# Kernel optimization log

Measured on AMD Instinct MI355X. Metric: run time of the kernel, lower is better.

## Reference

```python
import jax, jax.numpy as jnp
import numpy as np
import math

D = 256   # d_model / hidden_size
Q = 256   # q_num (query-side nodes)
K = 512   # k_num (key-side nodes)
NEG = -9e15


def _forward(q_enc, k_enc, rel_k, rel_v, k_adj,
             W_glob, b_glob, W_gv0, b_gv0, W_gv1, b_gv1,
             W_gq, b_gq, W_lq, b_lq,
             W_locgate, b_locgate, W_gate, b_gate):
    d = q_enc.shape[-1]
    scale = 1.0 / math.sqrt(d)
    act = jnp.tanh  # activation_func='tanh'

    # --- global sigmoid blending of k_enc with the mean query encoding ---
    q_glob_enc = jnp.mean(q_enc, axis=0)                       # [d]
    k_s = jax.nn.sigmoid((q_glob_enc @ W_glob + b_glob) @ k_enc.T * scale)  # [K]
    k_s = k_s[:, None]                                         # [K,1]
    g_1 = q_glob_enc @ W_gv0 + b_gv0                           # [d]
    k_1 = k_enc @ W_gv1 + b_gv1                                # [K,d]
    k_enc2 = (1.0 - k_s) * k_1 + k_s * g_1                     # [K,d]

    # --- global relation-aware attention over k nodes ---
    q_glob = q_enc @ W_gq + b_gq                               # [Q,d]
    qk_logit = q_glob @ k_enc2.T                               # [Q,K]
    qk_r = jnp.einsum('qd,qkd->qk', q_glob, rel_k)             # [Q,K]
    glob_attn = jax.nn.softmax(act((qk_logit + qk_r) * scale), axis=-1)  # [Q,K]

    # --- local adjacency-masked attention ---
    q_loc = q_enc @ W_lq + b_lq                                # [Q,d]
    qnk_logit = q_loc @ k_enc2.T                               # [Q,K]
    qnk_r = jnp.einsum('qd,qkd->qk', q_loc, rel_k)             # [Q,K]
    loc_attn = act((qnk_logit + qnk_r) * scale)                # [Q,K]
    # loc_weight_rep[q,i,j] = loc_attn[q,j]  (repeat + view in torch)
    mask = (k_adj != 0)[None, :, :]                            # [1,K,K]
    masked = jnp.where(mask, loc_attn[:, None, :], NEG)        # [Q,K,K]
    attn_adj_norm = jax.nn.softmax(masked, axis=-1)            # [Q,K,K]
    k_loc = jnp.einsum('qij,jd->qid', attn_adj_norm, k_enc2)   # [Q,K,d]

    # --- local gate between neighborhood value and self value ---
    # sigmoid(cat([k_loc, k_self]) @ W_locgate + b); k_self is broadcast k_enc2
    Wg1, Wg2 = W_locgate[:d], W_locgate[d:]                    # [d,1] each
    gate_logit = (jnp.einsum('qid,d->qi', k_loc, Wg1[:, 0])
                  + (k_enc2 @ Wg2)[None, :, 0] + b_locgate[0])  # [Q,K]
    loc_gate = jax.nn.sigmoid(gate_logit)[..., None]           # [Q,K,1]
    k_awr = loc_gate * k_loc + (1.0 - loc_gate) * k_enc2[None, :, :]  # [Q,K,d]

    # --- aggregate with global attention + relation values ---
    k_matmul = jnp.einsum('qk,qkd->qd', glob_attn, k_awr)      # [Q,d]
    k_r_matmul = jnp.einsum('qk,qkd->qd', glob_attn, rel_v)    # [Q,d]
    q_enc_new = k_matmul + k_r_matmul                          # [Q,d]

    # --- residual gate ---
    Wq1, Wq2 = W_gate[:d], W_gate[d:]
    gate = jax.nn.sigmoid(q_enc_new @ Wq1 + q_enc @ Wq2 + b_gate)  # [Q,1]
    h = gate * q_enc_new + (1.0 - gate) * q_enc                # [Q,d]
    return h


def setup_inputs() -> dict:
    key = jax.random.key(0)
    ks = jax.random.split(key, 16)
    def w(k, shape):
        return jax.random.normal(k, shape, jnp.float32) * 0.02
    return {
        'q_enc': jax.random.normal(ks[0], (Q, D), jnp.float32),
        'k_enc': jax.random.normal(ks[1], (K, D), jnp.float32),
        'rel_k': jax.random.normal(ks[2], (Q, K, D), jnp.float32) * 0.1,
        'rel_v': jax.random.normal(ks[3], (Q, K, D), jnp.float32) * 0.1,
        'k_adj': jax.random.randint(ks[4], (K, K), 0, 2, jnp.int64) if jax.config.jax_enable_x64 else jax.random.randint(ks[4], (K, K), 0, 2, jnp.int32),
        'W_glob': w(ks[5], (D, D)), 'b_glob': jnp.zeros((D,), jnp.float32),
        'W_gv0': w(ks[6], (D, D)), 'b_gv0': jnp.zeros((D,), jnp.float32),
        'W_gv1': w(ks[7], (D, D)), 'b_gv1': jnp.zeros((D,), jnp.float32),
        'W_gq': w(ks[8], (D, D)), 'b_gq': jnp.zeros((D,), jnp.float32),
        'W_lq': w(ks[9], (D, D)), 'b_lq': jnp.zeros((D,), jnp.float32),
        'W_locgate': w(ks[10], (2 * D, 1)), 'b_locgate': jnp.zeros((1,), jnp.float32),
        'W_gate': w(ks[11], (2 * D, 1)), 'b_gate': jnp.zeros((1,), jnp.float32),
    }


def reference(q_enc, k_enc, rel_k, rel_v, k_adj,
              W_glob, b_glob, W_gv0, b_gv0, W_gv1, b_gv1,
              W_gq, b_gq, W_lq, b_lq,
              W_locgate, b_locgate, W_gate, b_gate):
    return _forward(q_enc, k_enc, rel_k, rel_v, k_adj,
                    W_glob, b_glob, W_gv0, b_gv0, W_gv1, b_gv1,
                    W_gq, b_gq, W_lq, b_lq,
                    W_locgate, b_locgate, W_gate, b_gate)
```

## Files before the change

kernel.cpp:

```cpp
#include <hip/hip_runtime.h>
#include <math.h>

#define QN 256
#define KN 512
#define DN 256
#define SCALE 0.0625f

typedef __attribute__((ext_vector_type(8))) short short8v;
typedef __attribute__((ext_vector_type(4))) float f32x4;

__device__ __forceinline__ float sigf(float x){ return 1.0f/(1.0f+expf(-x)); }

__device__ __forceinline__ unsigned short f2bf(float x){
  unsigned u = __float_as_uint(x);
  unsigned r = (u + 0x7FFFu + ((u >> 16) & 1u)) >> 16;
  return (unsigned short)r;
}

__device__ __forceinline__ short8v ld8(const unsigned short* p){
  ushort4 a = *(const ushort4*)p;
  ushort4 b = *(const ushort4*)(p + 16);
  short8v r;
  r[0]=(short)a.x; r[1]=(short)a.y; r[2]=(short)a.z; r[3]=(short)a.w;
  r[4]=(short)b.x; r[5]=(short)b.y; r[6]=(short)b.z; r[7]=(short)b.w;
  return r;
}

__device__ __forceinline__ float wave_red(float v){
  #pragma unroll
  for (int off = 32; off; off >>= 1) v += __shfl_down(v, off);
  return v;
}

__global__ void kA2(const float* __restrict__ q_enc,
                    const float* __restrict__ W_glob, const float* __restrict__ W_gv0,
                    float* __restrict__ party0, float* __restrict__ party1){
  __shared__ float sm[256][9];
  __shared__ float qm[8];
  int b = blockIdx.x, t = threadIdx.x;
  int j0 = b*8;
  float4 lo = *(const float4*)(q_enc + (size_t)t*DN + j0);
  float4 hi = *(const float4*)(q_enc + (size_t)t*DN + j0 + 4);
  sm[t][0]=lo.x; sm[t][1]=lo.y; sm[t][2]=lo.z; sm[t][3]=lo.w;
  sm[t][4]=hi.x; sm[t][5]=hi.y; sm[t][6]=hi.z; sm[t][7]=hi.w;
  __syncthreads();
  #pragma unroll
  for (int s = 128; s > 0; s >>= 1){
    if (t < s){
      #pragma unroll
      for (int j = 0; j < 8; ++j) sm[t][j] += sm[t+s][j];
    }
    __syncthreads();
  }
  if (t < 8) qm[t] = sm[0][t] * (1.0f/QN);
  __syncthreads();
  float a0 = 0.f, a1 = 0.f;
  #pragma unroll
  for (int j = 0; j < 8; ++j){
    float s = qm[j];
    a0 = fmaf(s, W_glob[(size_t)(j0+j)*DN + t], a0);
    a1 = fmaf(s, W_gv0[(size_t)(j0+j)*DN + t], a1);
  }
  party0[b*256 + t] = a0; party1[b*256 + t] = a1;
}

__global__ void kA3(const float* __restrict__ party0, const float* __restrict__ party1,
                    const float* __restrict__ b_glob, const float* __restrict__ b_gv0,
                    float* __restrict__ tmp_glob, float* __restrict__ g1){
  int t = threadIdx.x;
  float a0 = b_glob[t], a1 = b_gv0[t];
  #pragma unroll
  for (int b = 0; b < 32; ++b){ a0 += party0[b*256 + t]; a1 += party1[b*256 + t]; }
  tmp_glob[t] = a0; g1[t] = a1;
}

__global__ void k23(const float* __restrict__ k_enc,
                    const float* __restrict__ W_gv1, const float* __restrict__ b_gv1,
                    const float* __restrict__ tmp_glob, const float* __restrict__ g1,
                    const float* __restrict__ W_locgate,
                    float* __restrict__ k_enc2, float* __restrict__ cvec,
                    float* __restrict__ gl2,
                    const float* __restrict__ q_enc,
                    const float* __restrict__ W_gq, const float* __restrict__ b_gq,
                    const float* __restrict__ W_lq, const float* __restrict__ b_lq,
                    float* __restrict__ q_glob, float* __restrict__ q_loc,
                    const int* __restrict__ kadj, unsigned short* __restrict__ mbf){
  __shared__ float sh1[256];
  __shared__ float red8[8];
  int bid = blockIdx.x, t = threadIdx.x;
  int w = t >> 6, lane = t & 63;
  int gid = bid*256 + t;
  if (gid < 65536){
    int4 v = ((const int4*)kadj)[gid];
    ushort4 o;
    o.x = v.x ? 0x3F80 : 0; o.y = v.y ? 0x3F80 : 0;
    o.z = v.z ? 0x3F80 : 0; o.w = v.w ? 0x3F80 : 0;
    ((ushort4*)mbf)[gid] = o;
  }
  if (bid < 512){
    int k = bid;
    float kv = k_enc[(size_t)k*DN + t];
    sh1[t] = kv;
    float part = wave_red(kv * tmp_glob[t]);
    if (lane == 0) red8[w] = part;
    __syncthreads();
    float dot = red8[0] + red8[1] + red8[2] + red8[3];
    float ks = sigf(dot * SCALE);
    float acc = b_gv1[t];
    #pragma unroll 8
    for (int j = 0; j < DN; ++j) acc = fmaf(sh1[j], W_gv1[(size_t)j*DN + t], acc);
    float v = (1.f - ks)*acc + ks*g1[t];
    k_enc2[(size_t)k*DN + t] = v;
    float pc = wave_red(v * W_locgate[t]);
    float pg = wave_red(v * W_locgate[DN + t]);
    __syncthreads();
    if (lane == 0){ red8[w] = pc; red8[4 + w] = pg; }
    __syncthreads();
    if (t == 0) cvec[k] = red8[0] + red8[1] + red8[2] + red8[3];
    if (t == 1) gl2[k]  = red8[4] + red8[5] + red8[6] + red8[7];
  } else {
    int q = bid - 512;
    sh1[t] = q_enc[(size_t)q*DN + t];
    __syncthreads();
    float a = b_gq[t], b = b_lq[t];
    #pragma unroll 8
    for (int j = 0; j < DN; ++j){
      float s = sh1[j];
      a = fmaf(s, W_gq[(size_t)j*DN + t], a);
      b = fmaf(s, W_lq[(size_t)j*DN + t], b);
    }
    q_glob[(size_t)q*DN + t] = a; q_loc[(size_t)q*DN + t] = b;
  }
}

__global__ void kb2(const float* __restrict__ rel_k,
                    const float* __restrict__ q_glob, const float* __restrict__ q_loc,
                    const float* __restrict__ ke2, const float* __restrict__ cvec,
                    float* __restrict__ exs, float* __restrict__ ev,
                    unsigned short* __restrict__ ebf, unsigned short* __restrict__ ecbf){
  int w = blockIdx.x*4 + (threadIdx.x >> 6);
  int lane = threadIdx.x & 63;
  int q = w >> 9, k = w & 511;
  float4 x = ((const float4*)(rel_k + (size_t)(q*KN + k)*DN))[lane];
  float4 a = ((const float4*)(q_glob + (size_t)q*DN))[lane];
  float4 b = ((const float4*)(q_loc  + (size_t)q*DN))[lane];
  float4 c = ((const float4*)(ke2    + (size_t)k*DN))[lane];
  float p1 = x.x*a.x + x.y*a.y + x.z*a.z + x.w*a.w;
  float p2 = x.x*b.x + x.y*b.y + x.z*b.z + x.w*b.w;
  float p3 = c.x*a.x + c.y*a.y + c.z*a.z + c.w*a.w;
  float p4 = c.x*b.x + c.y*b.y + c.z*b.z + c.w*b.w;
  #pragma unroll
  for (int off = 32; off; off >>= 1){
    p1 += __shfl_down(p1, off); p2 += __shfl_down(p2, off);
    p3 += __shfl_down(p3, off); p4 += __shfl_down(p4, off);
  }
  if (lane == 0){
    size_t idx = (size_t)q*KN + k;
    exs[idx] = expf(tanhf((p1 + p3)*SCALE));
    float evv = expf(tanhf((p2 + p4)*SCALE));
    ev[idx] = evv;
    ebf[idx] = f2bf(evv);
    ecbf[idx] = f2bf(evv * cvec[k]);
  }
}

__global__ __launch_bounds__(256) void kcA2m(const unsigned short* __restrict__ ebf,
                                             const unsigned short* __restrict__ ecbf,
                                             const unsigned short* __restrict__ mbf,
                                             const float* __restrict__ exs,
                                             const float* __restrict__ gl2,
                                             const float* __restrict__ blg_p,
                                             unsigned short* __restrict__ wvbf,
                                             float* __restrict__ v2){
  __shared__ unsigned short Ae[16*520];
  __shared__ unsigned short Ac[16*520];
  __shared__ unsigned short Bm[64*520];
  int t = threadIdx.x;
  int i0 = blockIdx.x*64, q0 = blockIdx.y*16;
  #pragma unroll
  for (int it = 0; it < 4; ++it){
    int c = t + 256*it; int row = c >> 6, col = (c & 63)*8;
    *(uint4*)&Ae[row*520 + col] = *(const uint4*)&ebf[(size_t)(q0+row)*KN + col];
    *(uint4*)&Ac[row*520 + col] = *(const uint4*)&ecbf[(size_t)(q0+row)*KN + col];
  }
  #pragma unroll
  for (int it = 0; it < 16; ++it){
    int c = t + 256*it; int row = c >> 6, col = (c & 63)*8;
    *(uint4*)&Bm[row*520 + col] = *(const uint4*)&mbf[(size_t)(i0+row)*KN + col];
  }
  __syncthreads();
  int w = t >> 6, l = t & 63;
  int g16 = l >> 4, l16 = l & 15;
  f32x4 aS = {0.f,0.f,0.f,0.f}, aN = {0.f,0.f,0.f,0.f};
  const unsigned short* pe = &Ae[l16*520];
  const unsigned short* pc = &Ac[l16*520];
  const unsigned short* pb = &Bm[(16*w + l16)*520];
  #pragma unroll
  for (int kk = 0; kk < 16; ++kk){
    int k0 = kk*32 + 4*g16;
    short8v fa = ld8(pe + k0);
    short8v fc = ld8(pc + k0);
    short8v fb = ld8(pb + k0);
    aS = __builtin_amdgcn_mfma_f32_16x16x32_bf16(fa, fb, aS, 0, 0, 0);
    aN = __builtin_amdgcn_mfma_f32_16x16x32_bf16(fc, fb, aN, 0, 0, 0);
  }
  float blg = blg_p[0];
  int i = i0 + 16*w + l16;
  float gli = gl2[i];
  #pragma unroll
  for (int r = 0; r < 4; ++r){
    int q = q0 + 4*g16 + r;
    size_t idx = (size_t)q*KN + i;
    float s = aS[r], n = aN[r];
    float lgv = sigf(n/s + gli + blg);
    float ex = exs[idx];
    wvbf[idx] = f2bf(ex*lgv/s);
    v2[idx] = ex*(1.f - lgv);
  }
}

__global__ __launch_bounds__(256) void kcC2m(const unsigned short* __restrict__ wvbf,
                                             const unsigned short* __restrict__ mbf,
                                             const float* __restrict__ ev,
                                             const float* __restrict__ v2,
                                             float* __restrict__ coef){
  __shared__ unsigned short Aw[16*520];
  __shared__ unsigned short Bm2[512*72];
  int t = threadIdx.x;
  int j0 = blockIdx.x*64, q0 = blockIdx.y*16;
  #pragma unroll
  for (int it = 0; it < 4; ++it){
    int c = t + 256*it; int row = c >> 6, col = (c & 63)*8;
    *(uint4*)&Aw[row*520 + col] = *(const uint4*)&wvbf[(size_t)(q0+row)*KN + col];
  }
  #pragma unroll
  for (int it = 0; it < 16; ++it){
    int c = t + 256*it; int row = c >> 3, col = (c & 7)*8;
    *(uint4*)&Bm2[row*72 + col] = *(const uint4*)&mbf[(size_t)row*KN + j0 + col];
  }
  __syncthreads();
  int w = t >> 6, l = t & 63;
  int g16 = l >> 4, l16 = l & 15;
  f32x4 aU = {0.f,0.f,0.f,0.f};
  const unsigned short* pa = &Aw[l16*520];
  int nn = 16*w + l16;
  #pragma unroll
  for (int kk = 0; kk < 16; ++kk){
    int k0 = kk*32 + 4*g16;
    short8v fa = ld8(pa + k0);
    short8v fb;
    #pragma unroll
    for (int e = 0; e < 4; ++e){
      fb[e]   = (short)Bm2[(k0+e)*72 + nn];
      fb[4+e] = (short)Bm2[(k0+16+e)*72 + nn];
    }
    aU = __builtin_amdgcn_mfma_f32_16x16x32_bf16(fa, fb, aU, 0, 0, 0);
  }
  int j = j0 + nn;
  #pragma unroll
  for (int r = 0; r < 4; ++r){
    int q = q0 + 4*g16 + r;
    size_t idx = (size_t)q*KN + j;
    coef[idx] = aU[r]*ev[idx] + v2[idx];
  }
}

__global__ __launch_bounds__(512) void kDE(const float* __restrict__ relv,
                                           const float* __restrict__ ke2,
                                           const float* __restrict__ exs,
                                           const float* __restrict__ coef,
                                           const float* __restrict__ q_enc,
                                           const float* __restrict__ W_gate,
                                           const float* __restrict__ b_gate,
                                           float* __restrict__ out){
  __shared__ float red[512];
  __shared__ float4 pacc[8][64];
  int q = blockIdx.x, t = threadIdx.x, w = t >> 6, lane = t & 63;
  red[t] = exs[(size_t)q*KN + t];
  __syncthreads();
  #pragma unroll
  for (int s = 256; s > 0; s >>= 1){
    if (t < s) red[t] += red[t+s];
    __syncthreads();
  }
  float invs = 1.0f / red[0];
  float4 acc = make_float4(0.f,0.f,0.f,0.f);
  int kbase = w*64;
  #pragma unroll 4
  for (int kk = 0; kk < 64; ++kk){
    int k = kbase + kk;
    float gk = exs[(size_t)q*KN + k];
    float ck = coef[(size_t)q*KN + k];
    float4 xv = ((const float4*)(relv + (size_t)(q*KN + k)*DN))[lane];
    float4 kv = ((const float4*)(ke2 + (size_t)k*DN))[lane];
    acc.x = fmaf(gk, xv.x, fmaf(ck, kv.x, acc.x));
    acc.y = fmaf(gk, xv.y, fmaf(ck, kv.y, acc.y));
    acc.z = fmaf(gk, xv.z, fmaf(ck, kv.z, acc.z));
    acc.w = fmaf(gk, xv.w, fmaf(ck, kv.w, acc.w));
  }
  pacc[w][lane] = acc;
  __syncthreads();
  if (t < 64){
    float4 r = pacc[0][t];
    #pragma unroll
    for (int w2 = 1; w2 < 8; ++w2){
      float4 p = pacc[w2][t];
      r.x += p.x; r.y += p.y; r.z += p.z; r.w += p.w;
    }
    r.x *= invs; r.y *= invs; r.z *= invs; r.w *= invs;
    float4 qe = ((const float4*)(q_enc + (size_t)q*DN))[t];
    float4 w1 = ((const float4*)(W_gate))[t];
    float4 w2v = ((const float4*)(W_gate + DN))[t];
    float pd = r.x*w1.x + r.y*w1.y + r.z*w1.z + r.w*w1.w
             + qe.x*w2v.x + qe.y*w2v.y + qe.z*w2v.z + qe.w*w2v.w;
    #pragma unroll
    for (int off = 32; off; off >>= 1) pd += __shfl_down(pd, off);
    float gate = sigf(__shfl(pd, 0) + b_gate[0]);
    float4 h;
    h.x = gate*r.x + (1.f-gate)*qe.x;
    h.y = gate*r.y + (1.f-gate)*qe.y;
    h.z = gate*r.z + (1.f-gate)*qe.z;
    h.w = gate*r.w + (1.f-gate)*qe.w;
    ((float4*)(out + (size_t)q*DN))[t] = h;
  }
}

extern "C" void kernel_launch(void* const* d_in, const int* in_sizes, int n_in,
                              void* d_out, int out_size, void* d_ws, size_t ws_size,
                              hipStream_t stream){
  const float* q_enc     = (const float*)d_in[0];
  const float* k_enc     = (const float*)d_in[1];
  const float* rel_k     = (const float*)d_in[2];
  const float* rel_v     = (const float*)d_in[3];
  const int*   k_adj     = (const int*)  d_in[4];
  const float* W_glob    = (const float*)d_in[5];
  const float* b_glob    = (const float*)d_in[6];
  const float* W_gv0     = (const float*)d_in[7];
  const float* b_gv0     = (const float*)d_in[8];
  const float* W_gv1     = (const float*)d_in[9];
  const float* b_gv1     = (const float*)d_in[10];
  const float* W_gq      = (const float*)d_in[11];
  const float* b_gq      = (const float*)d_in[12];
  const float* W_lq      = (const float*)d_in[13];
  const float* b_lq      = (const float*)d_in[14];
  const float* W_locgate = (const float*)d_in[15];
  const float* b_locgate = (const float*)d_in[16];
  const float* W_gate    = (const float*)d_in[17];
  const float* b_gate    = (const float*)d_in[18];
  float* out = (float*)d_out;

  float* ws = (float*)d_ws;
  float* party0   = ws;
  float* party1   = party0 + 8192;
  float* tmp_glob = party1 + 8192;
  float* g1       = tmp_glob + 256;
  float* k_enc2   = g1 + 256;
  float* cvec     = k_enc2 + 131072;
  float* gl2      = cvec + 512;
  float* q_glob   = gl2 + 512;
  float* q_loc    = q_glob + 65536;
  float* exs      = q_loc + 65536;
  float* evb      = exs + 131072;
  float* v2       = evb + 131072;
  float* coef     = v2 + 131072;
  unsigned short* mbf  = (unsigned short*)(coef + 131072);
  unsigned short* ebf  = mbf + 262144;
  unsigned short* ecbf = ebf + 131072;
  unsigned short* wvbf = ecbf + 131072;

  kA2<<<32, 256, 0, stream>>>(q_enc, W_glob, W_gv0, party0, party1);
  kA3<<<1, 256, 0, stream>>>(party0, party1, b_glob, b_gv0, tmp_glob, g1);
  k23<<<768, 256, 0, stream>>>(k_enc, W_gv1, b_gv1, tmp_glob, g1, W_locgate,
                               k_enc2, cvec, gl2,
                               q_enc, W_gq, b_gq, W_lq, b_lq, q_glob, q_loc,
                               k_adj, mbf);
  kb2<<<32768, 256, 0, stream>>>(rel_k, q_glob, q_loc, k_enc2, cvec,
                                 exs, evb, ebf, ecbf);
  kcA2m<<<dim3(8, 16), 256, 0, stream>>>(ebf, ecbf, mbf, exs, gl2, b_locgate, wvbf, v2);
  kcC2m<<<dim3(8, 16), 256, 0, stream>>>(wvbf, mbf, evb, v2, coef);
  kDE<<<256, 512, 0, stream>>>(rel_v, k_enc2, exs, coef, q_enc, W_gate, b_gate, out);
}
```

Baseline: 102.0 us.

## Fold kA3 reduction into k23, regroup kb2 work per wave, use nontemporal loads

Removes the single-block kA3 launch by having every k-block in k23 redundantly sum the 32 partial vectors plus biases. kb2 now has each 16-lane group handle one (q,k) pair over 4 iterations, so one wave covers four keys and the grid shrinks 4x. rel_k and rel_v are read with nontemporal loads to avoid polluting cache with the large streaming tensors, and kDE unrolls deeper. The trade-off is redundant reduction work in 512 blocks and fewer blocks in flight for kb2.

```diff
diff --git a/kernel.cpp b/kernel.cpp
--- a/kernel.cpp
+++ b/kernel.cpp
@@ -64,19 +64,10 @@
   party0[b*256 + t] = a0; party1[b*256 + t] = a1;
 }
 
-__global__ void kA3(const float* __restrict__ party0, const float* __restrict__ party1,
-                    const float* __restrict__ b_glob, const float* __restrict__ b_gv0,
-                    float* __restrict__ tmp_glob, float* __restrict__ g1){
-  int t = threadIdx.x;
-  float a0 = b_glob[t], a1 = b_gv0[t];
-  #pragma unroll
-  for (int b = 0; b < 32; ++b){ a0 += party0[b*256 + t]; a1 += party1[b*256 + t]; }
-  tmp_glob[t] = a0; g1[t] = a1;
-}
-
 __global__ void k23(const float* __restrict__ k_enc,
                     const float* __restrict__ W_gv1, const float* __restrict__ b_gv1,
-                    const float* __restrict__ tmp_glob, const float* __restrict__ g1,
+                    const float* __restrict__ party0, const float* __restrict__ party1,
+                    const float* __restrict__ b_glob, const float* __restrict__ b_gv0,
                     const float* __restrict__ W_locgate,
                     float* __restrict__ k_enc2, float* __restrict__ cvec,
                     float* __restrict__ gl2,
@@ -99,9 +90,15 @@
   }
   if (bid < 512){
     int k = bid;
+    float tg = b_glob[t], g1v = b_gv0[t];
+    #pragma unroll 8
+    for (int b2 = 0; b2 < 32; ++b2){
+      tg  += party0[b2*256 + t];
+      g1v += party1[b2*256 + t];
+    }
     float kv = k_enc[(size_t)k*DN + t];
     sh1[t] = kv;
-    float part = wave_red(kv * tmp_glob[t]);
+    float part = wave_red(kv * tg);
     if (lane == 0) red8[w] = part;
     __syncthreads();
     float dot = red8[0] + red8[1] + red8[2] + red8[3];
@@ -109,7 +106,7 @@
     float acc = b_gv1[t];
     #pragma unroll 8
     for (int j = 0; j < DN; ++j) acc = fmaf(sh1[j], W_gv1[(size_t)j*DN + t], acc);
-    float v = (1.f - ks)*acc + ks*g1[t];
+    float v = (1.f - ks)*acc + ks*g1v;
     k_enc2[(size_t)k*DN + t] = v;
     float pc = wave_red(v * W_locgate[t]);
     float pg = wave_red(v * W_locgate[DN + t]);
@@ -138,23 +135,31 @@
                     const float* __restrict__ ke2, const float* __restrict__ cvec,
                     float* __restrict__ exs, float* __restrict__ ev,
                     unsigned short* __restrict__ ebf, unsigned short* __restrict__ ecbf){
-  int w = blockIdx.x*4 + (threadIdx.x >> 6);
-  int lane = threadIdx.x & 63;
-  int q = w >> 9, k = w & 511;
-  float4 x = ((const float4*)(rel_k + (size_t)(q*KN + k)*DN))[lane];
-  float4 a = ((const float4*)(q_glob + (size_t)q*DN))[lane];
-  float4 b = ((const float4*)(q_loc  + (size_t)q*DN))[lane];
-  float4 c = ((const float4*)(ke2    + (size_t)k*DN))[lane];
-  float p1 = x.x*a.x + x.y*a.y + x.z*a.z + x.w*a.w;
-  float p2 = x.x*b.x + x.y*b.y + x.z*b.z + x.w*b.w;
-  float p3 = c.x*a.x + c.y*a.y + c.z*a.z + c.w*a.w;
-  float p4 = c.x*b.x + c.y*b.y + c.z*b.z + c.w*b.w;
-  #pragma unroll
-  for (int off = 32; off; off >>= 1){
+  int t = threadIdx.x;
+  int wv = t >> 6, lane = t & 63;
+  int g = lane >> 4, l16 = lane & 15;
+  int b = blockIdx.x;
+  int q = b >> 5;
+  int k = (b & 31)*16 + wv*4 + g;
+  float p1 = 0.f, p2 = 0.f, p3 = 0.f, p4 = 0.f;
+  #pragma unroll
+  for (int it = 0; it < 4; ++it){
+    int d = it*64 + l16*4;
+    f32x4 x  = __builtin_nontemporal_load((const f32x4*)(rel_k + ((size_t)q*KN + k)*DN + d));
+    float4 a  = *(const float4*)(q_glob + (size_t)q*DN + d);
+    float4 bb = *(const float4*)(q_loc  + (size_t)q*DN + d);
+    float4 c  = *(const float4*)(ke2    + (size_t)k*DN + d);
+    p1 += x[0]*a.x + x[1]*a.y + x[2]*a.z + x[3]*a.w;
+    p2 += x[0]*bb.x + x[1]*bb.y + x[2]*bb.z + x[3]*bb.w;
+    p3 += c.x*a.x + c.y*a.y + c.z*a.z + c.w*a.w;
+    p4 += c.x*bb.x + c.y*bb.y + c.z*bb.z + c.w*bb.w;
+  }
+  #pragma unroll
+  for (int off = 8; off; off >>= 1){
     p1 += __shfl_down(p1, off); p2 += __shfl_down(p2, off);
     p3 += __shfl_down(p3, off); p4 += __shfl_down(p4, off);
   }
-  if (lane == 0){
+  if (l16 == 0){
     size_t idx = (size_t)q*KN + k;
     exs[idx] = expf(tanhf((p1 + p3)*SCALE));
     float evv = expf(tanhf((p2 + p4)*SCALE));
@@ -286,17 +291,17 @@
   float invs = 1.0f / red[0];
   float4 acc = make_float4(0.f,0.f,0.f,0.f);
   int kbase = w*64;
-  #pragma unroll 4
+  #pragma unroll 8
   for (int kk = 0; kk < 64; ++kk){
     int k = kbase + kk;
     float gk = exs[(size_t)q*KN + k];
     float ck = coef[(size_t)q*KN + k];
-    float4 xv = ((const float4*)(relv + (size_t)(q*KN + k)*DN))[lane];
+    f32x4 xv = __builtin_nontemporal_load((const f32x4*)(relv + ((size_t)q*KN + k)*DN) + lane);
     float4 kv = ((const float4*)(ke2 + (size_t)k*DN))[lane];
-    acc.x = fmaf(gk, xv.x, fmaf(ck, kv.x, acc.x));
-    acc.y = fmaf(gk, xv.y, fmaf(ck, kv.y, acc.y));
-    acc.z = fmaf(gk, xv.z, fmaf(ck, kv.z, acc.z));
-    acc.w = fmaf(gk, xv.w, fmaf(ck, kv.w, acc.w));
+    acc.x = fmaf(gk, xv[0], fmaf(ck, kv.x, acc.x));
+    acc.y = fmaf(gk, xv[1], fmaf(ck, kv.y, acc.y));
+    acc.z = fmaf(gk, xv[2], fmaf(ck, kv.z, acc.z));
+    acc.w = fmaf(gk, xv[3], fmaf(ck, kv.w, acc.w));
   }
   pacc[w][lane] = acc;
   __syncthreads();
@@ -352,9 +357,7 @@
   float* ws = (float*)d_ws;
   float* party0   = ws;
   float* party1   = party0 + 8192;
-  float* tmp_glob = party1 + 8192;
-  float* g1       = tmp_glob + 256;
-  float* k_enc2   = g1 + 256;
+  float* k_enc2   = party1 + 8192;
   float* cvec     = k_enc2 + 131072;
   float* gl2      = cvec + 512;
   float* q_glob   = gl2 + 512;
@@ -369,13 +372,12 @@
   unsigned short* wvbf = ecbf + 131072;
 
   kA2<<<32, 256, 0, stream>>>(q_enc, W_glob, W_gv0, party0, party1);
-  kA3<<<1, 256, 0, stream>>>(party0, party1, b_glob, b_gv0, tmp_glob, g1);
-  k23<<<768, 256, 0, stream>>>(k_enc, W_gv1, b_gv1, tmp_glob, g1, W_locgate,
-                               k_enc2, cvec, gl2,
+  k23<<<768, 256, 0, stream>>>(k_enc, W_gv1, b_gv1, party0, party1, b_glob, b_gv0,
+                               W_locgate, k_enc2, cvec, gl2,
                                q_enc, W_gq, b_gq, W_lq, b_lq, q_glob, q_loc,
                                k_adj, mbf);
-  kb2<<<32768, 256, 0, stream>>>(rel_k, q_glob, q_loc, k_enc2, cvec,
-                                 exs, evb, ebf, ecbf);
+  kb2<<<8192, 256, 0, stream>>>(rel_k, q_glob, q_loc, k_enc2, cvec,
+                                exs, evb, ebf, ecbf);
   kcA2m<<<dim3(8, 16), 256, 0, stream>>>(ebf, ecbf, mbf, exs, gl2, b_locgate, wvbf, v2);
   kcC2m<<<dim3(8, 16), 256, 0, stream>>>(wvbf, mbf, evb, v2, coef);
   kDE<<<256, 512, 0, stream>>>(rel_v, k_enc2, exs, coef, q_enc, W_gate, b_gate, out);
```

Result: faster. 91.38 us (-10.4%).
